# Kernel tuning notes

Measured on AMD Instinct MI355X. Metric: run time of the kernel, lower is better.

## Reference

```python
import jax, jax.numpy as jnp
import numpy as np

DIM = 1024
NUM_HEADS = 16
HEAD_DIM = DIM // NUM_HEADS


def _xavier(key, shape):
    fan_out, fan_in = shape[0], shape[1]
    limit = float(np.sqrt(6.0 / (fan_in + fan_out)))
    return jax.random.uniform(key, shape, jnp.float32, -limit, limit)


def setup_inputs() -> dict:
    key = jax.random.key(0)
    k_x, k_in, k_out = jax.random.split(key, 3)
    x = jax.random.normal(k_x, (2, 2048, DIM), jnp.float32)
    in_proj_weight = _xavier(k_in, (3 * DIM, DIM))
    in_proj_bias = jnp.zeros((3 * DIM,), jnp.float32)
    out_proj_weight = _xavier(k_out, (DIM, DIM))
    out_proj_bias = jnp.zeros((DIM,), jnp.float32)
    return {
        "x": x,
        "in_proj_weight": in_proj_weight,
        "in_proj_bias": in_proj_bias,
        "out_proj_weight": out_proj_weight,
        "out_proj_bias": out_proj_bias,
    }


def reference(x, in_proj_weight, in_proj_bias, out_proj_weight, out_proj_bias):
    B, T, C = x.shape
    H, D = NUM_HEADS, HEAD_DIM
    # fused QKV projection: [B,T,3C]
    qkv = x @ in_proj_weight.T + in_proj_bias
    qkv = qkv.reshape(B, T, 3, H, D).transpose(2, 0, 3, 1, 4)  # [3,B,H,T,D]
    q, k, v = qkv[0], qkv[1], qkv[2]
    scale = 1.0 / jnp.sqrt(jnp.asarray(D, x.dtype))
    scores = jnp.einsum("bhqd,bhkd->bhqk", q, k) * scale  # [B,H,T,T]
    attn = jax.nn.softmax(scores, axis=-1)
    out = jnp.einsum("bhqk,bhkd->bhqd", attn, v)  # [B,H,T,D]
    out = out.transpose(0, 2, 1, 3).reshape(B, T, C)
    return out @ out_proj_weight.T + out_proj_bias
```

## Files before the change

### kernel.cpp

```cpp
#include <hip/hip_runtime.h>
#include <stdint.h>

typedef unsigned short bf16u;
typedef unsigned int u32;
typedef __attribute__((ext_vector_type(8))) short s16x8;
typedef __attribute__((ext_vector_type(4))) float f32x4;
typedef __attribute__((ext_vector_type(16))) float f32x16;
typedef __attribute__((ext_vector_type(2))) int i32x2;

#define QSCALE 0.18033688011112042f

static __device__ __forceinline__ bf16u f2bf(float f) {
    uint32_t u = __float_as_uint(f);
    uint32_t r = (u + 0x7FFFu + ((u >> 16) & 1u)) >> 16;
    return (bf16u)r;
}
static __device__ __forceinline__ u32 pack2(float lo, float hi) {
    return (u32)f2bf(lo) | ((u32)f2bf(hi) << 16);
}
static __device__ __forceinline__ u32 cvtpk(float lo, float hi) {
    u32 r;
    asm("v_cvt_pk_bf16_f32 %0, %1, %2" : "=v"(r) : "v"(lo), "v"(hi));
    return r;
}
static __device__ __forceinline__ i32x2 plswap(u32 x, u32 y) {
    return __builtin_amdgcn_permlane32_swap((int)x, (int)y, false, false);
}

static __device__ __forceinline__ f32x4 mfma16(s16x8 a, s16x8 b, f32x4 c) {
    return __builtin_amdgcn_mfma_f32_16x16x32_bf16(a, b, c, 0, 0, 0);
}
static __device__ __forceinline__ f32x16 mfma32(s16x8 a, s16x8 b, f32x16 c) {
    return __builtin_amdgcn_mfma_f32_32x32x16_bf16(a, b, c, 0, 0, 0);
}

#define GLDS(gsrc, ldst)                                                        \
    __builtin_amdgcn_global_load_lds(                                           \
        (const __attribute__((address_space(1))) void*)(gsrc),                  \
        (__attribute__((address_space(3))) void*)(ldst), 16, 0, 0)

__global__ __launch_bounds__(256) void cvt3_f32_bf16_kernel(
    const float* __restrict__ in0, bf16u* __restrict__ out0, int n0,
    const float* __restrict__ in1, bf16u* __restrict__ out1, int n1,
    const float* __restrict__ in2, bf16u* __restrict__ out2, int n2) {
    union Pack { bf16u h[8]; uint4 u; };
    const int step = gridDim.x * 256 * 8;
#define CVT_LOOP(inp, outp, n)                                                  \
    for (int i = (blockIdx.x * 256 + threadIdx.x) * 8; i < (n); i += step) {    \
        const float4 a = *(const float4*)((inp) + i);                           \
        const float4 b = *(const float4*)((inp) + i + 4);                       \
        Pack p;                                                                 \
        p.h[0] = f2bf(a.x); p.h[1] = f2bf(a.y); p.h[2] = f2bf(a.z);             \
        p.h[3] = f2bf(a.w); p.h[4] = f2bf(b.x); p.h[5] = f2bf(b.y);             \
        p.h[6] = f2bf(b.z); p.h[7] = f2bf(b.w);                                 \
        *(uint4*)((outp) + i) = p.u;                                            \
    }
    CVT_LOOP(in0, out0, n0)
    CVT_LOOP(in1, out1, n1)
    CVT_LOOP(in2, out2, n2)
#undef CVT_LOOP
}

template <int MODE, int RECTM, int RECTN>
__global__ __launch_bounds__(256) void gemm_bt_kernel(
    const bf16u* __restrict__ A, const bf16u* __restrict__ Bt,
    const float* __restrict__ bias, float* __restrict__ Cf,
    bf16u* __restrict__ Qo, bf16u* __restrict__ Ko, bf16u* __restrict__ Vto,
    int M, int N, int K) {
    __shared__ bf16u As[128 * 32];
    __shared__ bf16u Bs[128 * 32];
    const int tid  = threadIdx.x;
    const int wave = tid >> 6, lane = tid & 63;
    const int wr = wave >> 1, wc = wave & 1;
    const int ri = lane & 15, hi = lane >> 4;

    const int id  = blockIdx.x + blockIdx.y * gridDim.x;
    const int xcd = id & 7, rr = id >> 3;
    const int nrm = gridDim.x / RECTM;
    const int m0 = ((xcd % nrm) * RECTM + (rr % RECTM)) * 128;
    const int n0 = ((xcd / nrm) * RECTN + (rr / RECTM)) * 128;

    f32x4 acc[4][4];
#pragma unroll
    for (int i = 0; i < 4; ++i)
#pragma unroll
        for (int j = 0; j < 4; ++j) acc[i][j] = (f32x4){0.f, 0.f, 0.f, 0.f};

    for (int k0 = 0; k0 < K; k0 += 32) {
        __syncthreads();
#pragma unroll
        for (int it = 0; it < 2; ++it) {
            const int chunk = it * 4 + wave;
            const int e = chunk * 512 + lane * 8;
            const int r = e >> 5, c = e & 31;
            GLDS(A  + (size_t)(m0 + r) * K + (k0 + c), As + chunk * 512);
            GLDS(Bt + (size_t)(n0 + r) * K + (k0 + c), Bs + chunk * 512);
        }
        __syncthreads();
        s16x8 af[4], bfr[4];
#pragma unroll
        for (int i = 0; i < 4; ++i) {
            af[i]  = *(const s16x8*)(As + (wr * 64 + i * 16 + ri) * 32 + hi * 8);
            bfr[i] = *(const s16x8*)(Bs + (wc * 64 + i * 16 + ri) * 32 + hi * 8);
        }
#pragma unroll
        for (int i = 0; i < 4; ++i)
#pragma unroll
            for (int j = 0; j < 4; ++j) acc[i][j] = mfma16(af[i], bfr[j], acc[i][j]);
    }

#pragma unroll
    for (int i = 0; i < 4; ++i) {
#pragma unroll
        for (int j = 0; j < 4; ++j) {
#pragma unroll
            for (int r = 0; r < 4; ++r) {
                const int row = m0 + wr * 64 + i * 16 + hi * 4 + r;
                const int col = n0 + wc * 64 + j * 16 + ri;
                const float v = acc[i][j][r] + bias[col];
                if constexpr (MODE == 0) {
                    Cf[(size_t)row * N + col] = v;
                } else {
                    const int which = col >> 10, h = (col >> 6) & 15, d = col & 63;
                    const int b = row >> 11, t = row & 2047;
                    const int bh = b * 16 + h;
                    if (which == 2) {
                        Vto[(((size_t)bh) * 64 + d) * 2048 + t] = f2bf(v);
                    } else if (which == 0) {
                        Qo[(((size_t)bh) * 2048 + t) * 64 + d] = f2bf(v * QSCALE);
                    } else {
                        Ko[(((size_t)bh) * 2048 + t) * 64 + d] = f2bf(v);
                    }
                }
            }
        }
    }
}

__global__ __launch_bounds__(512) void attn_kernel(
    const bf16u* __restrict__ Q, const bf16u* __restrict__ K,
    const bf16u* __restrict__ Vt, bf16u* __restrict__ O) {
    __shared__ uint4 smem4[4 * 64 * 72 * 2 / 16];
    bf16u* Ks0 = (bf16u*)smem4;
    bf16u* Vs0 = Ks0 + 64 * 72;
    bf16u* Ks1 = Vs0 + 64 * 72;
    bf16u* Vs1 = Ks1 + 64 * 72;
    float* mrg = (float*)smem4;

    const int tid = threadIdx.x, lane = tid & 63;
    const int wave = tid >> 6, wg = wave & 3, kvh = wave >> 2;
    const int ri = lane & 31, hi = lane >> 5;

    const int id  = blockIdx.x + blockIdx.y * gridDim.x;
    const int xcd = id & 7, rr = id >> 3;
    const int bh = xcd * 4 + (rr >> 4);
    const int bq = rr & 15;

    const int b = bh >> 4, h = bh & 15;
    const int q0 = bq * 128 + wg * 32;
    const bf16u* Qb = Q  + (size_t)bh * 2048 * 64;
    const bf16u* Kb = K  + (size_t)bh * 2048 * 64;
    const bf16u* Vb = Vt + (size_t)bh * 64 * 2048;

    s16x8 qf[4];
#pragma unroll
    for (int c = 0; c < 4; ++c)
        qf[c] = *(const s16x8*)(Qb + (size_t)(q0 + ri) * 64 + c * 16 + hi * 8);

    const bf16u* Ksh = kvh ? Ks1 : Ks0;
    const bf16u* Vsh = kvh ? Vs1 : Vs0;

    f32x16 oacc[2];
#pragma unroll
    for (int r = 0; r < 16; ++r) { oacc[0][r] = 0.f; oacc[1][r] = 0.f; }
    float m = -1e30f, lsum = 0.f;

    const int srow = tid >> 3, sc = tid & 7;
    for (int kt = 0; kt < 16; ++kt) {
        const uint4 k0 = *(const uint4*)(Kb + (size_t)(kt * 64 + srow) * 64 + sc * 8);
        const uint4 k1 = *(const uint4*)(Kb + (size_t)((kt + 16) * 64 + srow) * 64 + sc * 8);
        const uint4 v0 = *(const uint4*)(Vb + (size_t)srow * 2048 + kt * 64 + sc * 8);
        const uint4 v1 = *(const uint4*)(Vb + (size_t)srow * 2048 + (kt + 16) * 64 + sc * 8);
        __syncthreads();
        *(uint4*)(Ks0 + srow * 72 + sc * 8) = k0;
        *(uint4*)(Ks1 + srow * 72 + sc * 8) = k1;
        *(uint4*)(Vs0 + srow * 72 + sc * 8) = v0;
        *(uint4*)(Vs1 + srow * 72 + sc * 8) = v1;
        __syncthreads();

        f32x16 sa[2];
#pragma unroll
        for (int r = 0; r < 16; ++r) { sa[0][r] = 0.f; sa[1][r] = 0.f; }
#pragma unroll
        for (int kb2 = 0; kb2 < 2; ++kb2) {
            const int row = kb2 * 32 + ri;
#pragma unroll
            for (int c = 0; c < 4; ++c) {
                s16x8 kf = *(const s16x8*)(Ksh + row * 72 + (2 * c + hi) * 8);
                sa[kb2] = mfma32(kf, qf[c], sa[kb2]);
            }
        }

        float pmt[16];
#pragma unroll
        for (int r = 0; r < 16; ++r) pmt[r] = fmaxf(sa[0][r], sa[1][r]);
#pragma unroll
        for (int s = 8; s > 0; s >>= 1)
#pragma unroll
            for (int r = 0; r < s; ++r) pmt[r] = fmaxf(pmt[r], pmt[r + s]);
        const float pm = fmaxf(pmt[0], __shfl_xor(pmt[0], 32));

        if (!__all(pm <= m + 8.f)) {
            const float mn = fmaxf(m, pm);
            const float al = __builtin_amdgcn_exp2f(m - mn);
            m = mn;
            lsum *= al;
#pragma unroll
            for (int r = 0; r < 16; ++r) { oacc[0][r] *= al; oacc[1][r] *= al; }
        }

        float rs0 = 0.f, rs1 = 0.f, rs2 = 0.f, rs3 = 0.f;
#pragma unroll
        for (int kb2 = 0; kb2 < 2; ++kb2)
#pragma unroll
            for (int r = 0; r < 16; ++r) {
                const float p = __builtin_amdgcn_exp2f(sa[kb2][r] - m);
                sa[kb2][r] = p;
                if ((r & 3) == 0) rs0 += p;
                else if ((r & 3) == 1) rs1 += p;
                else if ((r & 3) == 2) rs2 += p;
                else rs3 += p;
            }
        float rs = (rs0 + rs1) + (rs2 + rs3);
        rs += __shfl_xor(rs, 32);
        lsum += rs;

        s16x8 pb[4];
#pragma unroll
        for (int blk = 0; blk < 2; ++blk) {
            u32 pk[4][2];
#pragma unroll
            for (int j = 0; j < 4; ++j) {
                pk[j][0] = cvtpk(sa[blk][4 * j + 0], sa[blk][4 * j + 1]);
                pk[j][1] = cvtpk(sa[blk][4 * j + 2], sa[blk][4 * j + 3]);
            }
#pragma unroll
            for (int halfq = 0; halfq < 2; ++halfq) {
                const int ja = 2 * halfq, jb = ja + 1;
                const i32x2 s0 = plswap(pk[ja][0], pk[jb][0]);
                const i32x2 s1 = plswap(pk[ja][1], pk[jb][1]);
                union { u32 w[4]; s16x8 v; } pu;
                pu.w[0] = (u32)s0.x;
                pu.w[1] = (u32)s1.x;
                pu.w[2] = (u32)s0.y;
                pu.w[3] = (u32)s1.y;
                pb[blk * 2 + halfq] = pu.v;
            }
        }

#pragma unroll
        for (int dt = 0; dt < 2; ++dt) {
            const int row = dt * 32 + ri;
#pragma unroll
            for (int k4 = 0; k4 < 4; ++k4) {
                s16x8 vf = *(const s16x8*)(Vsh + row * 72 + (2 * k4 + hi) * 8);
                oacc[dt] = mfma32(vf, pb[k4], oacc[dt]);
            }
        }
    }

    __syncthreads();
    if (kvh) {
        float* p = mrg + (wg * 64 + lane) * 35;
        p[0] = m; p[1] = lsum;
#pragma unroll
        for (int r = 0; r < 16; ++r) { p[2 + r] = oacc[0][r]; p[18 + r] = oacc[1][r]; }
    }
    __syncthreads();
    if (!kvh) {
        const float* p = mrg + (wg * 64 + lane) * 35;
        const float m1 = p[0], l1 = p[1];
        const float mn = fmaxf(m, m1);
        const float a0 = __builtin_amdgcn_exp2f(m - mn);
        const float a1 = __builtin_amdgcn_exp2f(m1 - mn);
        const float inv = 1.f / (lsum * a0 + l1 * a1);
        const int t = q0 + ri;
        bf16u* Ob = O + ((size_t)b * 2048 + t) * 1024 + h * 64;
#pragma unroll
        for (int dt = 0; dt < 2; ++dt)
#pragma unroll
            for (int j = 0; j < 4; ++j) {
                const int d0 = dt * 32 + j * 8 + hi * 4;
                const float e0 = (oacc[dt][4 * j + 0] * a0 + p[2 + dt * 16 + 4 * j + 0] * a1) * inv;
                const float e1 = (oacc[dt][4 * j + 1] * a0 + p[2 + dt * 16 + 4 * j + 1] * a1) * inv;
                const float e2 = (oacc[dt][4 * j + 2] * a0 + p[2 + dt * 16 + 4 * j + 2] * a1) * inv;
                const float e3 = (oacc[dt][4 * j + 3] * a0 + p[2 + dt * 16 + 4 * j + 3] * a1) * inv;
                uint2 wv; wv.x = pack2(e0, e1); wv.y = pack2(e2, e3);
                *(uint2*)(Ob + d0) = wv;
            }
    }
}

extern "C" void kernel_launch(void* const* d_in, const int* in_sizes, int n_in,
                              void* d_out, int out_size, void* d_ws, size_t ws_size,
                              hipStream_t stream) {
    const float* x     = (const float*)d_in[0];
    const float* w_in  = (const float*)d_in[1];
    const float* b_in  = (const float*)d_in[2];
    const float* w_out = (const float*)d_in[3];
    const float* b_out = (const float*)d_in[4];
    float* out = (float*)d_out;

    char* ws = (char*)d_ws;
    bf16u* xb    = (bf16u*)(ws);
    bf16u* wqkvb = (bf16u*)(ws + 8388608);
    bf16u* woutb = (bf16u*)(ws + 14680064);
    bf16u* qb    = (bf16u*)(ws + 16777216);
    bf16u* kb    = (bf16u*)(ws + 25165824);
    bf16u* vtb   = (bf16u*)(ws + 33554432);
    bf16u* attnb = xb;

    cvt3_f32_bf16_kernel<<<2048, 256, 0, stream>>>(
        x, xb, 4096 * 1024, w_in, wqkvb, 3072 * 1024, w_out, woutb, 1024 * 1024);

    gemm_bt_kernel<1, 8, 12><<<dim3(32, 24), 256, 0, stream>>>(
        xb, wqkvb, b_in, nullptr, qb, kb, vtb, 4096, 3072, 1024);

    attn_kernel<<<dim3(16, 32), 512, 0, stream>>>(qb, kb, vtb, attnb);

    gemm_bt_kernel<0, 8, 4><<<dim3(32, 8), 256, 0, stream>>>(
        attnb, woutb, b_out, out, nullptr, nullptr, nullptr, 4096, 1024, 1024);
}
```

Baseline: 133.8 us.

## Double-buffer LDS tiles in GEMM to overlap global loads with MFMA

Splits the GEMM's shared-memory A/B tiles into two ping-pong buffers. The next K-slice is issued as a direct global-to-LDS load while the MFMAs consume the current slice, and one barrier per step is removed. This hides global memory latency in the QKV and output projections, at the cost of doubling LDS use per block, which may lower occupancy. It assumes K is a multiple of 64.

```diff
diff --git a/kernel.cpp b/kernel.cpp
--- a/kernel.cpp
+++ b/kernel.cpp
@@ -67,8 +67,10 @@
     const float* __restrict__ bias, float* __restrict__ Cf,
     bf16u* __restrict__ Qo, bf16u* __restrict__ Ko, bf16u* __restrict__ Vto,
     int M, int N, int K) {
-    __shared__ bf16u As[128 * 32];
-    __shared__ bf16u Bs[128 * 32];
+    __shared__ bf16u As0[128 * 32];
+    __shared__ bf16u Bs0[128 * 32];
+    __shared__ bf16u As1[128 * 32];
+    __shared__ bf16u Bs1[128 * 32];
     const int tid  = threadIdx.x;
     const int wave = tid >> 6, lane = tid & 63;
     const int wr = wave >> 1, wc = wave & 1;
@@ -86,28 +88,45 @@
 #pragma unroll
         for (int j = 0; j < 4; ++j) acc[i][j] = (f32x4){0.f, 0.f, 0.f, 0.f};
 
-    for (int k0 = 0; k0 < K; k0 += 32) {
+#define STAGE(Ad, Bd, k0)                                                       \
+    _Pragma("unroll")                                                           \
+    for (int it = 0; it < 2; ++it) {                                            \
+        const int chunk = it * 4 + wave;                \
+        const int e = chunk * 512 + lane * 8;                                   \
+        const int r = e >> 5, c = e & 31;                                       \
+        GLDS(A  + (size_t)(m0 + r) * K + ((k0) + c), (Ad) + chunk * 512);       \
+        GLDS(Bt + (size_t)(n0 + r) * K + ((k0) + c), (Bd) + chunk * 512);       \
+    }
+
+#define KSTEP(Asrc, Bsrc)                                                       \
+    {                                                                           \
+        s16x8 af[4], bfr[4];                                                    \
+        _Pragma("unroll")                                                       \
+        for (int i = 0; i < 4; ++i) {                                           \
+            af[i]  = *(const s16x8*)((Asrc) + (wr * 64 + i * 16 + ri) * 32 + hi * 8); \
+            bfr[i] = *(const s16x8*)((Bsrc) + (wc * 64 + i * 16 + ri) * 32 + hi * 8); \
+        }                                                                       \
+        _Pragma("unroll")                                                       \
+        for (int i = 0; i < 4; ++i)                                             \
+            _Pragma("unroll")                                                   \
+            for (int j = 0; j < 4; ++j) acc[i][j] = mfma16(af[i], bfr[j], acc[i][j]); \
+    }
+
+    STAGE(As0, Bs0, 0)
+    __syncthreads();
+
+    const int T = K >> 5;
+    for (int t2 = 0; t2 < (T >> 1); ++t2) {
+        const int t = t2 * 2;
+        STAGE(As1, Bs1, (t + 1) * 32)
+        KSTEP(As0, Bs0)
         __syncthreads();
-#pragma unroll
-        for (int it = 0; it < 2; ++it) {
-            const int chunk = it * 4 + wave;
-            const int e = chunk * 512 + lane * 8;
-            const int r = e >> 5, c = e & 31;
-            GLDS(A  + (size_t)(m0 + r) * K + (k0 + c), As + chunk * 512);
-            GLDS(Bt + (size_t)(n0 + r) * K + (k0 + c), Bs + chunk * 512);
-        }
+        if (t + 2 < T) { STAGE(As0, Bs0, (t + 2) * 32) }
+        KSTEP(As1, Bs1)
         __syncthreads();
-        s16x8 af[4], bfr[4];
-#pragma unroll
-        for (int i = 0; i < 4; ++i) {
-            af[i]  = *(const s16x8*)(As + (wr * 64 + i * 16 + ri) * 32 + hi * 8);
-            bfr[i] = *(const s16x8*)(Bs + (wc * 64 + i * 16 + ri) * 32 + hi * 8);
-        }
-#pragma unroll
-        for (int i = 0; i < 4; ++i)
-#pragma unroll
-            for (int j = 0; j < 4; ++j) acc[i][j] = mfma16(af[i], bfr[j], acc[i][j]);
-    }
+    }
+#undef STAGE
+#undef KSTEP
 
 #pragma unroll
     for (int i = 0; i < 4; ++i) {
```

Result: no change. 132.0 us (-1.4%).
